# Performance work log

Measured on AMD Instinct MI355X. Metric: run time of the kernel, lower is better.

The kernel has to match this reference:

```python
import jax, jax.numpy as jnp
import numpy as np

ALPHA = 0.2          # LeakyReLU negative slope
MASK_VAL = -9e15     # zero_vec value from the torch code
COS_EPS = 1e-8       # torch cosine_similarity default eps


def gat_forward_relation(src, dst, rel, W, b, adj):
    # src: [N,D], dst/rel: [N,K,D], adj: [N,K] (int mask), W: [2D,D], b: [D]
    N, K, D = dst.shape
    a_input = jnp.concatenate(
        [jnp.broadcast_to(src[:, None, :], (N, K, D)), dst], axis=-1)  # [N,K,2D]
    h = jnp.einsum('nke,ed->nkd', a_input, W) + b                      # fc
    # cosine similarity along last dim (torch eps semantics)
    num = jnp.sum(h * rel, axis=-1)                                    # [N,K]
    den = (jnp.maximum(jnp.sqrt(jnp.sum(h * h, axis=-1)), COS_EPS) *
           jnp.maximum(jnp.sqrt(jnp.sum(rel * rel, axis=-1)), COS_EPS))
    e = num / den
    e = jnp.where(e > 0, e, ALPHA * e)                                 # LeakyReLU
    e = jnp.where(adj > 0, e, MASK_VAL)                                # mask
    att = jax.nn.softmax(e, axis=1)                                    # over K
    agg = jnp.einsum('nk,nkd->nd', att, dst)                           # bmm
    return agg + src                                                   # concat=False: no ELU


def setup_inputs() -> dict:
    key = jax.random.key(0)
    ks = jax.random.split(key, 6)
    N, K, D = 8192, 32, 128
    return {
        'src_embs': jax.random.normal(ks[0], (N, D), dtype=jnp.float32),
        'dst_embs': jax.random.normal(ks[1], (N, K, D), dtype=jnp.float32),
        'relations': jax.random.normal(ks[2], (N, K, D), dtype=jnp.float32),
        'W_fc': jax.random.normal(ks[3], (2 * D, D), dtype=jnp.float32) / np.sqrt(2 * D),
        'b_fc': jnp.zeros((D,), dtype=jnp.float32),
        'adj': jax.random.randint(ks[4], (N, K), 0, 2, dtype=jnp.int32),
    }


def reference(src_embs, dst_embs, relations, W_fc, b_fc, adj):
    # KGAT loop body applies the GAT layer twice (dropout is eval no-op)
    x = gat_forward_relation(src_embs, dst_embs, relations, W_fc, b_fc, adj)
    x = gat_forward_relation(x, dst_embs, relations, W_fc, b_fc, adj)
    return x
```

## Files before the change

kernel.cpp:

```cpp
#include <hip/hip_runtime.h>
#include <math.h>

constexpr int NN = 8192;
constexpr int K  = 32;
constexpr int D  = 128;
constexpr int DP = D + 4;
constexpr float ALPHA = 0.2f;
constexpr float MASKV = -9e15f;
constexpr float EPS   = 1e-8f;

typedef __bf16 bf16x8 __attribute__((ext_vector_type(8)));
typedef float  f32x4  __attribute__((ext_vector_type(4)));

__device__ __forceinline__ float dot4(const float4 a, const float4 b) {
    return fmaf(a.x, b.x, fmaf(a.y, b.y, fmaf(a.z, b.z, a.w * b.w)));
}

__global__ __launch_bounds__(256) void conv_w(const float* __restrict__ W,
                                              __bf16* __restrict__ whi,
                                              __bf16* __restrict__ wlo) {
    const int idx = blockIdx.x * 256 + threadIdx.x;
    const int j = idx & 7, l = (idx >> 3) & 63, nt = (idx >> 9) & 7, s = idx >> 12;
    const int e = 32 * s + 8 * (l >> 4) + j;
    const int c = 16 * nt + (l & 15);
    const float x = W[(size_t)(D + e) * D + c];
    const __bf16 h = (__bf16)x;
    whi[idx] = h;
    wlo[idx] = (__bf16)(x - (float)h);
}

__global__ __launch_bounds__(256) void gat_fused(
    const float* __restrict__ src,
    const float* __restrict__ dst,
    const float* __restrict__ rel,
    const float* __restrict__ W,
    const float* __restrict__ b,
    const int*   __restrict__ adj,
    const __bf16* __restrict__ whi,
    const __bf16* __restrict__ wlo,
    float* __restrict__ out)
{
    __shared__ __align__(16) float dst_s[K * DP];
    __shared__ __align__(16) float rel_s[K * DP];
    __shared__ __align__(16) float hd_s [K * DP];
    __shared__ __align__(16) float x_s [D];
    __shared__ __align__(16) float sW_s[D];
    __shared__ __align__(16) float sWp[2 * D];
    __shared__ __align__(16) float b_s[D];
    __shared__ float e_s[K], att_s[K], A_s[K], B_s[K], R_s[K];
    __shared__ int   adj_s[K];

    const int n  = blockIdx.x;
    const int t  = threadIdx.x;
    const int w  = t >> 6;
    const int l  = t & 63;
    const int lr = l & 15;
    const int lk = l >> 4;

    const float* dstn = dst + (size_t)n * K * D;
    const float* reln = rel + (size_t)n * K * D;

    if (t < 32)       ((float4*)x_s)[t]      = ((const float4*)(src + (size_t)n * D))[t];
    else if (t < 64)  ((float4*)b_s)[t - 32] = ((const float4*)b)[t - 32];
    else if (t < 96)  adj_s[t - 64] = adj[n * K + (t - 64)];
    #pragma unroll
    for (int jj = 0; jj < 4; ++jj) {
        const int idx = t + 256 * jj;
        const int row = idx >> 5, col = idx & 31;
        *(float4*)(dst_s + row * DP + 4 * col) = ((const float4*)dstn)[idx];
        *(float4*)(rel_s + row * DP + 4 * col) = ((const float4*)reln)[idx];
    }
    __syncthreads();

    {
        f32x4 acc00 = {0,0,0,0}, acc01 = {0,0,0,0};
        f32x4 acc10 = {0,0,0,0}, acc11 = {0,0,0,0};
        #pragma unroll
        for (int ks = 0; ks < 4; ++ks) {
            const int cb = 32 * ks + 8 * lk;
            bf16x8 ah0, al0, ah1, al1;
            {
                const float* p0 = dst_s + lr * DP + cb;
                const float* p1 = dst_s + (16 + lr) * DP + cb;
                const f32x4 x0 = *(const f32x4*)p0, x1 = *(const f32x4*)(p0 + 4);
                const f32x4 y0 = *(const f32x4*)p1, y1 = *(const f32x4*)(p1 + 4);
                #pragma unroll
                for (int jj = 0; jj < 4; ++jj) {
                    float v; __bf16 h;
                    v = x0[jj]; h = (__bf16)v; ah0[jj]     = h; al0[jj]     = (__bf16)(v - (float)h);
                    v = x1[jj]; h = (__bf16)v; ah0[4 + jj] = h; al0[4 + jj] = (__bf16)(v - (float)h);
                    v = y0[jj]; h = (__bf16)v; ah1[jj]     = h; al1[jj]     = (__bf16)(v - (float)h);
                    v = y1[jj]; h = (__bf16)v; ah1[4 + jj] = h; al1[4 + jj] = (__bf16)(v - (float)h);
                }
            }
            #pragma unroll
            for (int ni = 0; ni < 2; ++ni) {
                const int nt = 2 * w + ni;
                const size_t fo = (size_t)((ks * 8 + nt) * 64 + l) * 8;
                const bf16x8 bh = *(const bf16x8*)(whi + fo);
                const bf16x8 bl = *(const bf16x8*)(wlo + fo);
                f32x4& a0 = ni ? acc10 : acc00;
                f32x4& a1 = ni ? acc11 : acc01;
                a0 = __builtin_amdgcn_mfma_f32_16x16x32_bf16(ah0, bh, a0, 0, 0, 0);
                a0 = __builtin_amdgcn_mfma_f32_16x16x32_bf16(ah0, bl, a0, 0, 0, 0);
                a0 = __builtin_amdgcn_mfma_f32_16x16x32_bf16(al0, bh, a0, 0, 0, 0);
                a1 = __builtin_amdgcn_mfma_f32_16x16x32_bf16(ah1, bh, a1, 0, 0, 0);
                a1 = __builtin_amdgcn_mfma_f32_16x16x32_bf16(ah1, bl, a1, 0, 0, 0);
                a1 = __builtin_amdgcn_mfma_f32_16x16x32_bf16(al1, bh, a1, 0, 0, 0);
            }
        }
        #pragma unroll
        for (int ni = 0; ni < 2; ++ni) {
            const int nt = 2 * w + ni;
            const float bc = b_s[16 * nt + lr];
            const f32x4 a0 = ni ? acc10 : acc00;
            const f32x4 a1 = ni ? acc11 : acc01;
            #pragma unroll
            for (int r = 0; r < 4; ++r) {
                hd_s[(4 * lk + r) * DP + 16 * nt + lr]      = a0[r] + bc;
                hd_s[(16 + 4 * lk + r) * DP + 16 * nt + lr] = a1[r] + bc;
            }
        }
    }

    {
        const int dd = t & (D - 1), eh = t >> 7;
        float acc = 0.f;
        const float* Wt = W + (size_t)(64 * eh) * D + dd;
        #pragma unroll 8
        for (int e = 0; e < 64; ++e)
            acc = fmaf(x_s[64 * eh + e], Wt[(size_t)e * D], acc);
        sWp[eh * D + dd] = acc;
    }
    __syncthreads();
    if (t < D) sW_s[t] = sWp[t] + sWp[D + t];
    __syncthreads();

    const int kc = 8 * w + (l & 7);
    const int q  = l >> 3;

    {
        float a_ = 0.f, bb = 0.f, r2 = 0.f, sr = 0.f, sh = 0.f, ss = 0.f;
        #pragma unroll
        for (int jj = 0; jj < 4; ++jj) {
            const int f = q + 8 * jj;
            const float4 rv = *(const float4*)(rel_s + kc * DP + 4 * f);
            const float4 hv = *(const float4*)(hd_s + kc * DP + 4 * f);
            const float4 sv = ((const float4*)sW_s)[f];
            a_ += dot4(hv, rv);  bb += dot4(hv, hv);  r2 += dot4(rv, rv);
            sr += dot4(sv, rv);  sh += dot4(sv, hv);  ss += dot4(sv, sv);
        }
        #pragma unroll
        for (int m = 8; m < 64; m <<= 1) {
            a_ += __shfl_xor(a_, m);  bb += __shfl_xor(bb, m);
            r2 += __shfl_xor(r2, m);  sr += __shfl_xor(sr, m);
            sh += __shfl_xor(sh, m);  ss += __shfl_xor(ss, m);
        }
        if (q == 0) {
            const float R   = fmaxf(sqrtf(r2), EPS);
            const float hh  = ss + 2.f * sh + bb;
            const float den = fmaxf(sqrtf(hh), EPS) * R;
            float e = (sr + a_) / den;
            e = e > 0.f ? e : ALPHA * e;
            if (adj_s[kc] <= 0) e = MASKV;
            e_s[kc] = e;  A_s[kc] = a_;  B_s[kc] = bb;  R_s[kc] = R;
        }
    }
    __syncthreads();

    if (t < K) {
        float v = e_s[t], m = v;
        #pragma unroll
        for (int s = 16; s > 0; s >>= 1) m = fmaxf(m, __shfl_xor(m, s));
        const float p = expf(v - m);
        float sm = p;
        #pragma unroll
        for (int s = 16; s > 0; s >>= 1) sm += __shfl_xor(sm, s);
        att_s[t] = p / sm;
    }
    __syncthreads();

    if (t < D) {
        float agg = 0.f;
        #pragma unroll
        for (int k = 0; k < K; ++k) agg = fmaf(att_s[k], dst_s[k * DP + t], agg);
        x_s[t] = agg + x_s[t];
    }
    __syncthreads();

    {
        const int dd = t & (D - 1), eh = t >> 7;
        float acc = 0.f;
        const float* Wt = W + (size_t)(64 * eh) * D + dd;
        #pragma unroll 8
        for (int e = 0; e < 64; ++e)
            acc = fmaf(x_s[64 * eh + e], Wt[(size_t)e * D], acc);
        sWp[eh * D + dd] = acc;
    }
    __syncthreads();
    if (t < D) sW_s[t] = sWp[t] + sWp[D + t];
    __syncthreads();

    {
        float sr = 0.f, sh = 0.f, ss = 0.f;
        #pragma unroll
        for (int jj = 0; jj < 4; ++jj) {
            const int f = q + 8 * jj;
            const float4 rv = *(const float4*)(rel_s + kc * DP + 4 * f);
            const float4 hv = *(const float4*)(hd_s + kc * DP + 4 * f);
            const float4 sv = ((const float4*)sW_s)[f];
            sr += dot4(sv, rv);  sh += dot4(sv, hv);  ss += dot4(sv, sv);
        }
        #pragma unroll
        for (int m = 8; m < 64; m <<= 1) {
            sr += __shfl_xor(sr, m);  sh += __shfl_xor(sh, m);  ss += __shfl_xor(ss, m);
        }
        if (q == 0) {
            const float hh  = ss + 2.f * sh + B_s[kc];
            const float den = fmaxf(sqrtf(hh), EPS) * R_s[kc];
            float e = (sr + A_s[kc]) / den;
            e = e > 0.f ? e : ALPHA * e;
            if (adj_s[kc] <= 0) e = MASKV;
            e_s[kc] = e;
        }
    }
    __syncthreads();

    if (t < K) {
        float v = e_s[t], m = v;
        #pragma unroll
        for (int s = 16; s > 0; s >>= 1) m = fmaxf(m, __shfl_xor(m, s));
        const float p = expf(v - m);
        float sm = p;
        #pragma unroll
        for (int s = 16; s > 0; s >>= 1) sm += __shfl_xor(sm, s);
        att_s[t] = p / sm;
    }
    __syncthreads();

    if (t < D) {
        float agg = 0.f;
        #pragma unroll
        for (int k = 0; k < K; ++k) agg = fmaf(att_s[k], dst_s[k * DP + t], agg);
        out[(size_t)n * D + t] = agg + x_s[t];
    }
}

extern "C" void kernel_launch(void* const* d_in, const int* in_sizes, int n_in,
                              void* d_out, int out_size, void* d_ws, size_t ws_size,
                              hipStream_t stream) {
    const float* src = (const float*)d_in[0];
    const float* dst = (const float*)d_in[1];
    const float* rel = (const float*)d_in[2];
    const float* W   = (const float*)d_in[3];
    const float* b   = (const float*)d_in[4];
    const int*   adj = (const int*)d_in[5];
    float* out = (float*)d_out;

    __bf16* whi = (__bf16*)d_ws;
    __bf16* wlo = whi + 4 * 8 * 64 * 8;

    conv_w<<<64, 256, 0, stream>>>(W, whi, wlo);
    gat_fused<<<NN, 256, 0, stream>>>(src, dst, rel, W, b, adj, whi, wlo, out);
}
```

Before: 379.5 us.

## Double block size to 512 threads and redistribute per-node work across eight waves

```diff
diff --git a/kernel.cpp b/kernel.cpp
--- a/kernel.cpp
+++ b/kernel.cpp
@@ -29,7 +29,7 @@
     wlo[idx] = (__bf16)(x - (float)h);
 }
 
-__global__ __launch_bounds__(256) void gat_fused(
+__global__ __launch_bounds__(512) void gat_fused(
     const float* __restrict__ src,
     const float* __restrict__ dst,
     const float* __restrict__ rel,
@@ -45,7 +45,7 @@
     __shared__ __align__(16) float hd_s [K * DP];
     __shared__ __align__(16) float x_s [D];
     __shared__ __align__(16) float sW_s[D];
-    __shared__ __align__(16) float sWp[2 * D];
+    __shared__ __align__(16) float sWp[4 * D];
     __shared__ __align__(16) float b_s[D];
     __shared__ float e_s[K], att_s[K], A_s[K], B_s[K], R_s[K];
     __shared__ int   adj_s[K];
@@ -64,17 +64,29 @@
     else if (t < 64)  ((float4*)b_s)[t - 32] = ((const float4*)b)[t - 32];
     else if (t < 96)  adj_s[t - 64] = adj[n * K + (t - 64)];
     #pragma unroll
-    for (int jj = 0; jj < 4; ++jj) {
-        const int idx = t + 256 * jj;
+    for (int jj = 0; jj < 2; ++jj) {
+        const int idx = t + 512 * jj;
         const int row = idx >> 5, col = idx & 31;
         *(float4*)(dst_s + row * DP + 4 * col) = ((const float4*)dstn)[idx];
         *(float4*)(rel_s + row * DP + 4 * col) = ((const float4*)reln)[idx];
     }
-    __syncthreads();
-
-    {
-        f32x4 acc00 = {0,0,0,0}, acc01 = {0,0,0,0};
-        f32x4 acc10 = {0,0,0,0}, acc11 = {0,0,0,0};
+    {
+        const int dd = t & 127, es = t >> 7;
+        const float* srcp = src + (size_t)n * D + 32 * es;
+        const float* Wp   = W + (size_t)(32 * es) * D + dd;
+        float acc = 0.f;
+        #pragma unroll 8
+        for (int e = 0; e < 32; ++e)
+            acc = fmaf(srcp[e], Wp[(size_t)e * D], acc);
+        sWp[es * D + dd] = acc;
+    }
+    __syncthreads();
+
+    if (t < D) sW_s[t] = (sWp[t] + sWp[D + t]) + (sWp[2 * D + t] + sWp[3 * D + t]);
+    __syncthreads();
+
+    {
+        f32x4 acc0 = {0,0,0,0}, acc1 = {0,0,0,0};
         #pragma unroll
         for (int ks = 0; ks < 4; ++ks) {
             const int cb = 32 * ks + 8 * lk;
@@ -93,57 +105,33 @@
                     v = y1[jj]; h = (__bf16)v; ah1[4 + jj] = h; al1[4 + jj] = (__bf16)(v - (float)h);
                 }
             }
-            #pragma unroll
-            for (int ni = 0; ni < 2; ++ni) {
-                const int nt = 2 * w + ni;
-                const size_t fo = (size_t)((ks * 8 + nt) * 64 + l) * 8;
-                const bf16x8 bh = *(const bf16x8*)(whi + fo);
-                const bf16x8 bl = *(const bf16x8*)(wlo + fo);
-                f32x4& a0 = ni ? acc10 : acc00;
-                f32x4& a1 = ni ? acc11 : acc01;
-                a0 = __builtin_amdgcn_mfma_f32_16x16x32_bf16(ah0, bh, a0, 0, 0, 0);
-                a0 = __builtin_amdgcn_mfma_f32_16x16x32_bf16(ah0, bl, a0, 0, 0, 0);
-                a0 = __builtin_amdgcn_mfma_f32_16x16x32_bf16(al0, bh, a0, 0, 0, 0);
-                a1 = __builtin_amdgcn_mfma_f32_16x16x32_bf16(ah1, bh, a1, 0, 0, 0);
-                a1 = __builtin_amdgcn_mfma_f32_16x16x32_bf16(ah1, bl, a1, 0, 0, 0);
-                a1 = __builtin_amdgcn_mfma_f32_16x16x32_bf16(al1, bh, a1, 0, 0, 0);
-            }
-        }
-        #pragma unroll
-        for (int ni = 0; ni < 2; ++ni) {
-            const int nt = 2 * w + ni;
-            const float bc = b_s[16 * nt + lr];
-            const f32x4 a0 = ni ? acc10 : acc00;
-            const f32x4 a1 = ni ? acc11 : acc01;
-            #pragma unroll
-            for (int r = 0; r < 4; ++r) {
-                hd_s[(4 * lk + r) * DP + 16 * nt + lr]      = a0[r] + bc;
-                hd_s[(16 + 4 * lk + r) * DP + 16 * nt + lr] = a1[r] + bc;
-            }
-        }
-    }
-
-    {
-        const int dd = t & (D - 1), eh = t >> 7;
-        float acc = 0.f;
-        const float* Wt = W + (size_t)(64 * eh) * D + dd;
-        #pragma unroll 8
-        for (int e = 0; e < 64; ++e)
-            acc = fmaf(x_s[64 * eh + e], Wt[(size_t)e * D], acc);
-        sWp[eh * D + dd] = acc;
-    }
-    __syncthreads();
-    if (t < D) sW_s[t] = sWp[t] + sWp[D + t];
-    __syncthreads();
-
-    const int kc = 8 * w + (l & 7);
-    const int q  = l >> 3;
+            const size_t fo = (size_t)((ks * 8 + w) * 64 + l) * 8;
+            const bf16x8 bh = *(const bf16x8*)(whi + fo);
+            const bf16x8 bl = *(const bf16x8*)(wlo + fo);
+            acc0 = __builtin_amdgcn_mfma_f32_16x16x32_bf16(ah0, bh, acc0, 0, 0, 0);
+            acc0 = __builtin_amdgcn_mfma_f32_16x16x32_bf16(ah0, bl, acc0, 0, 0, 0);
+            acc0 = __builtin_amdgcn_mfma_f32_16x16x32_bf16(al0, bh, acc0, 0, 0, 0);
+            acc1 = __builtin_amdgcn_mfma_f32_16x16x32_bf16(ah1, bh, acc1, 0, 0, 0);
+            acc1 = __builtin_amdgcn_mfma_f32_16x16x32_bf16(ah1, bl, acc1, 0, 0, 0);
+            acc1 = __builtin_amdgcn_mfma_f32_16x16x32_bf16(al1, bh, acc1, 0, 0, 0);
+        }
+        const float bc = b_s[16 * w + lr];
+        #pragma unroll
+        for (int r = 0; r < 4; ++r) {
+            hd_s[(4 * lk + r) * DP + 16 * w + lr]      = acc0[r] + bc;
+            hd_s[(16 + 4 * lk + r) * DP + 16 * w + lr] = acc1[r] + bc;
+        }
+    }
+    __syncthreads();
+
+    const int kc = 4 * w + (l & 3);
+    const int q2 = l >> 2;
 
     {
         float a_ = 0.f, bb = 0.f, r2 = 0.f, sr = 0.f, sh = 0.f, ss = 0.f;
         #pragma unroll
-        for (int jj = 0; jj < 4; ++jj) {
-            const int f = q + 8 * jj;
+        for (int it = 0; it < 2; ++it) {
+            const int f = q2 + 16 * it;
             const float4 rv = *(const float4*)(rel_s + kc * DP + 4 * f);
             const float4 hv = *(const float4*)(hd_s + kc * DP + 4 * f);
             const float4 sv = ((const float4*)sW_s)[f];
@@ -151,12 +139,12 @@
             sr += dot4(sv, rv);  sh += dot4(sv, hv);  ss += dot4(sv, sv);
         }
         #pragma unroll
-        for (int m = 8; m < 64; m <<= 1) {
+        for (int m = 4; m < 64; m <<= 1) {
             a_ += __shfl_xor(a_, m);  bb += __shfl_xor(bb, m);
             r2 += __shfl_xor(r2, m);  sr += __shfl_xor(sr, m);
             sh += __shfl_xor(sh, m);  ss += __shfl_xor(ss, m);
         }
-        if (q == 0) {
+        if (q2 == 0) {
             const float R   = fmaxf(sqrtf(r2), EPS);
             const float hh  = ss + 2.f * sh + bb;
             const float den = fmaxf(sqrtf(hh), EPS) * R;
@@ -189,33 +177,34 @@
     __syncthreads();
 
     {
-        const int dd = t & (D - 1), eh = t >> 7;
+        const int dd = t & 127, es = t >> 7;
+        const float* Wp = W + (size_t)(32 * es) * D + dd;
         float acc = 0.f;
-        const float* Wt = W + (size_t)(64 * eh) * D + dd;
         #pragma unroll 8
-        for (int e = 0; e < 64; ++e)
-            acc = fmaf(x_s[64 * eh + e], Wt[(size_t)e * D], acc);
-        sWp[eh * D + dd] = acc;
-    }
-    __syncthreads();
-    if (t < D) sW_s[t] = sWp[t] + sWp[D + t];
+        for (int e = 0; e < 32; ++e)
+            acc = fmaf(x_s[32 * es + e], Wp[(size_t)e * D], acc);
+        sWp[es * D + dd] = acc;
+    }
+    __syncthreads();
+
+    if (t < D) sW_s[t] = (sWp[t] + sWp[D + t]) + (sWp[2 * D + t] + sWp[3 * D + t]);
     __syncthreads();
 
     {
         float sr = 0.f, sh = 0.f, ss = 0.f;
         #pragma unroll
-        for (int jj = 0; jj < 4; ++jj) {
-            const int f = q + 8 * jj;
+        for (int it = 0; it < 2; ++it) {
+            const int f = q2 + 16 * it;
             const float4 rv = *(const float4*)(rel_s + kc * DP + 4 * f);
             const float4 hv = *(const float4*)(hd_s + kc * DP + 4 * f);
             const float4 sv = ((const float4*)sW_s)[f];
             sr += dot4(sv, rv);  sh += dot4(sv, hv);  ss += dot4(sv, sv);
         }
         #pragma unroll
-        for (int m = 8; m < 64; m <<= 1) {
+        for (int m = 4; m < 64; m <<= 1) {
             sr += __shfl_xor(sr, m);  sh += __shfl_xor(sh, m);  ss += __shfl_xor(ss, m);
         }
-        if (q == 0) {
+        if (q2 == 0) {
             const float hh  = ss + 2.f * sh + B_s[kc];
             const float den = fmaxf(sqrtf(hh), EPS) * R_s[kc];
             float e = (sr + A_s[kc]) / den;
@@ -261,5 +250,5 @@
     __bf16* wlo = whi + 4 * 8 * 64 * 8;
 
     conv_w<<<64, 256, 0, stream>>>(W, whi, wlo);
-    gat_fused<<<NN, 256, 0, stream>>>(src, dst, rel, W, b, adj, whi, wlo, out);
-}
+    gat_fused<<<NN, 512, 0, stream>>>(src, dst, rel, W, b, adj, whi, wlo, out);
+}
```

New measurement: 373.8 us. About the same (-1.5%).
